# Optimization experiments

Measured on AMD Instinct MI355X. Metric: run time of the kernel, lower is better.

The kernel has to match this reference:

```python
import jax, jax.numpy as jnp
import numpy as np

B, C, Cs, CI, H, W = 4, 256, 256, 128, 64, 64

def setup_inputs() -> dict:
    key = jax.random.key(0)
    ks = jax.random.split(key, 9)
    sq = 1.0 / np.sqrt(C)
    ss = 1.0 / np.sqrt(Cs)
    return {
        "x_main": jax.random.normal(ks[0], (B, C, H, W), jnp.float32),
        "z_p": jax.random.normal(ks[1], (B, Cs, H, W), jnp.float32),
        "Wq": jax.random.normal(ks[2], (CI, C), jnp.float32) * sq,
        "bq": jax.random.normal(ks[3], (CI,), jnp.float32) * 0.01,
        "Wk": jax.random.normal(ks[4], (CI, Cs), jnp.float32) * ss,
        "bk": jax.random.normal(ks[5], (CI,), jnp.float32) * 0.01,
        "Wv": jax.random.normal(ks[6], (C, Cs), jnp.float32) * ss,
        "bv": jax.random.normal(ks[7], (C,), jnp.float32) * 0.01,
        "gamma": jax.random.normal(ks[8], (1,), jnp.float32) * 0.1,
    }

def reference(x_main, z_p, Wq, bq, Wk, bk, Wv, bv, gamma):
    b, c, h, w = x_main.shape
    n = h * w
    xm = x_main.reshape(b, c, n)          # [B, C, N]
    zf = z_p.reshape(b, z_p.shape[1], n)  # [B, Cs, M] (M == N here)
    # 1x1 convs == per-pixel channel projections
    q = jnp.einsum('oc,bcn->bon', Wq, xm) + bq[None, :, None]  # [B, CI, N]
    k = jnp.einsum('oc,bcm->bom', Wk, zf) + bk[None, :, None]  # [B, CI, M]
    v = jnp.einsum('oc,bcm->bom', Wv, zf) + bv[None, :, None]  # [B, C, M]
    # energy[b, n, m] = q_n . k_m  (no scaling, as in the original)
    energy = jnp.einsum('bcn,bcm->bnm', q, k)
    attention = jax.nn.softmax(energy, axis=-1)
    out = jnp.einsum('bom,bnm->bon', v, attention)  # [B, C, N]
    out = out.reshape(b, c, h, w)
    return gamma * out + x_main
```

## Files before the change

### kernel.cpp

```cpp
#include <hip/hip_runtime.h>
#include <hip/hip_bf16.h>


typedef __bf16  bf16x8  __attribute__((ext_vector_type(8)));
typedef float   f32x16  __attribute__((ext_vector_type(16)));

#define LOG2E 1.4426950408889634f

union BF8 { __hip_bfloat162 h[4]; bf16x8 v; };
union U4  { unsigned u[4]; bf16x8 v; };

__device__ inline bf16x8 pack8(const float f[8]) {
  BF8 u;
#pragma unroll
  for (int i = 0; i < 4; i++)
    u.h[i] = __float22bfloat162_rn(float2{f[2 * i], f[2 * i + 1]});
  return u.v;
}

__device__ inline void dma16(const void* g, void* l) {
  __builtin_amdgcn_global_load_lds(
      (const __attribute__((address_space(1))) unsigned int*)g,
      (__attribute__((address_space(3))) unsigned int*)l, 16, 0, 0);
}

__global__ __launch_bounds__(256) void prep_kernel(
    const float* __restrict__ x, const float* __restrict__ z,
    const float* __restrict__ Wq, const float* __restrict__ Wk,
    const float* __restrict__ Wv,
    __hip_bfloat16* __restrict__ xf, __hip_bfloat16* __restrict__ zf,
    __hip_bfloat16* __restrict__ wfr)
{
  __shared__ float lds[256 * 65];
  const int bi = blockIdx.x;
  const int tid = threadIdx.x;
  if (bi < 512) {
    const int sel = bi >> 8;
    const int b   = (bi >> 6) & 3;
    const int pc  = bi & 63;
    const float* in = sel ? z : x;
    __hip_bfloat16* outp = sel ? zf : xf;
    const size_t ib = (size_t)b * 256 * 4096 + pc * 64;
#pragma unroll 4
    for (int r = 0; r < 64; r++) {
      int ch = r * 4 + (tid >> 6);
      lds[ch * 65 + (tid & 63)] = in[ib + (size_t)ch * 4096 + (tid & 63)];
    }
    __syncthreads();
    const size_t ob = ((size_t)(b * 128 + pc * 2)) * 8192;
#pragma unroll
    for (int i = 0; i < 8; i++) {
      int c = i * 256 + tid;
      int grp = c >> 10, cs = (c >> 6) & 15, rem = c & 63;
      int hf = rem >> 5, l32 = rem & 31;
      float f[8];
      int chb = cs * 16 + hf * 8;
#pragma unroll
      for (int j = 0; j < 8; j++)
        f[j] = lds[(chb + j) * 65 + grp * 32 + l32];
      *(bf16x8*)(outp + ob + grp * 8192 + cs * 512 + hf * 256 + l32 * 8) =
          pack8(f);
    }
  } else {
    const int base = (bi - 512) * 4096;
#pragma unroll
    for (int i = 0; i < 16; i++) {
      int c = base + i * 256 + tid;
      const float* Ws; __hip_bfloat16* dst; int rc;
      if (c < 4096)      { Ws = Wq; dst = wfr;          rc = c; }
      else if (c < 8192) { Ws = Wk; dst = wfr + 32768;  rc = c - 4096; }
      else               { Ws = Wv; dst = wfr + 65536;  rc = c - 8192; }
      int ot = rc >> 10, cs = (rc >> 6) & 15, rem = rc & 63;
      int hf = rem >> 5, l32 = rem & 31;
      const float* src = Ws + (ot * 32 + l32) * 256 + cs * 16 + hf * 8;
      float f[8];
#pragma unroll
      for (int j = 0; j < 8; j++) f[j] = src[j];
      *(bf16x8*)(dst + ot * 8192 + cs * 512 + hf * 256 + l32 * 8) = pack8(f);
    }
  }
}

__global__ __launch_bounds__(256, 2) void proj_mfma(
    const __hip_bfloat16* __restrict__ xf, const __hip_bfloat16* __restrict__ zf,
    const __hip_bfloat16* __restrict__ wfr,
    const float* __restrict__ bq, const float* __restrict__ bk,
    const float* __restrict__ bv,
    __hip_bfloat16* __restrict__ qp, __hip_bfloat16* __restrict__ kp,
    __hip_bfloat16* __restrict__ vp)
{
  const int bi = blockIdx.x;
  int mode, b, pc, h = 0;
  if (bi < 256) { mode = bi >> 7; b = (bi >> 5) & 3; pc = bi & 31; }
  else { int j = bi - 256; mode = 2; b = j >> 6; pc = (j >> 1) & 31; h = j & 1; }
  const int tid = threadIdx.x, w = tid >> 6, lane = tid & 63,
            l32 = lane & 31, half = lane >> 5;

  const __hip_bfloat16* X = (mode == 0) ? xf : zf;
  const int wtile = (mode == 2 ? h * 4 : 0) + w;
  const int wbase = (mode == 0) ? 0 : (mode == 1) ? 32768 : 65536;
  const __hip_bfloat16* wp = wfr + wbase + wtile * 8192 + lane * 8;
  bf16x8 wfg[16];
#pragma unroll
  for (int cs = 0; cs < 16; cs++) wfg[cs] = *(const bf16x8*)(wp + cs * 512);

  const float* bias = (mode == 0) ? bq : (mode == 1) ? bk : bv;
  const int ochb = (mode == 2 ? h * 128 : 0) + w * 32;
  float bb[16];
#pragma unroll
  for (int r = 0; r < 16; r++)
    bb[r] = bias[ochb + (r & 3) + 8 * (r >> 2) + 4 * half];

  const int t4 = (l32 >> 2) & 3;
  const int kperm = (t4 == 1 || t4 == 2) ? (l32 ^ 12) : l32;

#pragma unroll 1
  for (int it = 0; it < 4; it++) {
    const int pg = pc * 4 + it;
    const __hip_bfloat16* xb = X + ((size_t)(b * 128 + pg)) * 8192 + lane * 8;
    f32x16 O = {};
#pragma unroll
    for (int cs = 0; cs < 16; cs++) {
      bf16x8 xr = *(const bf16x8*)(xb + cs * 512);
      O = __builtin_amdgcn_mfma_f32_32x32x16_bf16(wfg[cs], xr, O, 0, 0, 0);
    }
    if (mode == 0) {
      __hip_bfloat16* qb = qp + ((size_t)(b * 128 + pg)) * 4096;
#pragma unroll
      for (int r = 0; r < 16; r++) {
        int oc = ochb + (r & 3) + 8 * (r >> 2) + 4 * half;
        qb[(oc >> 4) * 512 + ((oc >> 3) & 1) * 256 + l32 * 8 + (oc & 7)] =
            __float2bfloat16((O[r] + bb[r]) * LOG2E);
      }
    } else if (mode == 1) {
      __hip_bfloat16* kb = kp + ((size_t)(b * 128 + pg)) * 4096;
#pragma unroll
      for (int r = 0; r < 16; r++) {
        int oc = ochb + (r & 3) + 8 * (r >> 2) + 4 * half;
        kb[(oc >> 4) * 512 + ((oc >> 3) & 1) * 256 + kperm * 8 + (oc & 7)] =
            __float2bfloat16(O[r] + bb[r]);
      }
    } else {
      __hip_bfloat16* vb = vp + ((size_t)(b * 128 + pg)) * 8192
          + (h * 4 + w) * 1024 + (l32 >> 4) * 512 + ((l32 >> 3) & 1) * 256
          + (l32 & 7);
#pragma unroll
      for (int r = 0; r < 16; r++) {
        int rr = (r & 3) + 8 * (r >> 2) + 4 * half;
        vb[rr * 8] = __float2bfloat16(O[r] + bb[r]);
      }
    }
  }
}

struct AttnSmem {
  union {
    __hip_bfloat16 kbuf[2][8192];
    float ostage[256][33];
  } u;
  float redu[4][32];
  float rinv[32];
};

__global__ __launch_bounds__(256, 3) void attn_kernel(
    const __hip_bfloat16* __restrict__ qv, const __hip_bfloat16* __restrict__ kv,
    const __hip_bfloat16* __restrict__ vv,
    const float* __restrict__ x_main, const float* __restrict__ gammap,
    float* __restrict__ out)
{
  __shared__ AttnSmem sm;
  const int i  = blockIdx.x;
  const int b  = (i & 7) >> 1;
  const int qt = ((i >> 3) << 1) | (i & 1);
  const int n0 = qt * 32;
  const int tid  = threadIdx.x;
  const int w    = tid >> 6, lane = tid & 63, l32 = lane & 31;
  const int kh   = w >> 1, chh = w & 1;

  bf16x8 qf[8];
  {
    const __hip_bfloat16* qb = qv + ((size_t)(b * 128 + qt)) * 4096 + lane * 8;
#pragma unroll
    for (int cs = 0; cs < 8; cs++) qf[cs] = *(const bf16x8*)(qb + cs * 512);
  }

  const __hip_bfloat16* kg = kv + (size_t)(b * 128) * 4096;
  const __hip_bfloat16* vg = vv + (size_t)(b * 128) * 8192;

  auto stage = [&](int t) {
    __hip_bfloat16* kd = sm.u.kbuf[t & 1];
    const __hip_bfloat16* ksrc = kg + (size_t)t * 8192 + lane * 8;
#pragma unroll
    for (int c = 0; c < 4; c++) {
      int ck = w * 4 + c;
      dma16(ksrc + ck * 512, kd + ck * 512 + lane * 8);
    }
  };

  f32x16 Oacc[4];
#pragma unroll
  for (int c = 0; c < 4; c++)
#pragma unroll
    for (int r = 0; r < 16; r++) Oacc[c][r] = 0.f;

  float l_lane = 0.f;

  auto qk_tile = [&](int t) -> f32x16 {
    const __hip_bfloat16* kbase = sm.u.kbuf[t & 1] + kh * 4096 + lane * 8;
    f32x16 S = {};
#pragma unroll
    for (int cs = 0; cs < 8; cs++) {
      bf16x8 kf = *(const bf16x8*)(kbase + cs * 512);
      S = __builtin_amdgcn_mfma_f32_32x32x16_bf16(kf, qf[cs], S, 0, 0, 0);
    }
    return S;
  };

  auto pv_tile = [&](int t, const f32x16& S) {
    unsigned p2[8];
    float s0 = 0.f, s1 = 0.f;
#pragma unroll
    for (int i2 = 0; i2 < 8; i2++) {
      float a = exp2f(S[2 * i2]     - 64.0f);
      float c = exp2f(S[2 * i2 + 1] - 64.0f);
      if (i2 & 1) s1 += a + c; else s0 += a + c;
      union { __hip_bfloat162 h; unsigned u; } cv;
      cv.h = __float22bfloat162_rn(float2{a, c});
      p2[i2] = cv.u;
    }
    l_lane += s0 + s1;
    U4 f0, f1;
    f0.u[0] = p2[0]; f0.u[1] = p2[1]; f0.u[2] = p2[2]; f0.u[3] = p2[3];
    f1.u[0] = p2[4]; f1.u[1] = p2[5]; f1.u[2] = p2[6]; f1.u[3] = p2[7];
    const bf16x8 pf0 = f0.v, pf1 = f1.v;
    const __hip_bfloat16* vb = vg + (size_t)(t * 2 + kh) * 8192
                             + chh * 4096 + lane * 8;
#pragma unroll
    for (int c = 0; c < 4; c++) {
      bf16x8 v0 = *(const bf16x8*)(vb + c * 1024);
      Oacc[c] = __builtin_amdgcn_mfma_f32_32x32x16_bf16(v0, pf0, Oacc[c], 0, 0, 0);
      bf16x8 v1 = *(const bf16x8*)(vb + c * 1024 + 512);
      Oacc[c] = __builtin_amdgcn_mfma_f32_32x32x16_bf16(v1, pf1, Oacc[c], 0, 0, 0);
    }
  };

  stage(0);
  __syncthreads();
  stage(1);
  {
    f32x16 S = qk_tile(0);
    pv_tile(0, S);
  }
#pragma unroll 1
  for (int t = 1; t < 64; ++t) {
    __syncthreads();
    if (t < 63) stage(t + 1);
    f32x16 S = qk_tile(t);
    pv_tile(t, S);
  }

  float lfull = l_lane + __shfl_xor(l_lane, 32);
  if (lane < 32) sm.redu[w][l32] = lfull;
  __syncthreads();
  const int hb = lane >> 5;
  if (kh == 0) {
#pragma unroll
    for (int c = 0; c < 4; c++) {
#pragma unroll
      for (int r = 0; r < 16; r++) {
        int ch = (chh * 4 + c) * 32 + (r & 3) + 8 * (r >> 2) + 4 * hb;
        sm.u.ostage[ch][l32] = Oacc[c][r];
      }
    }
  }
  if (tid < 32) sm.rinv[tid] = 1.0f / (sm.redu[0][tid] + sm.redu[2][tid]);
  __syncthreads();
  if (kh == 1) {
#pragma unroll
    for (int c = 0; c < 4; c++) {
#pragma unroll
      for (int r = 0; r < 16; r++) {
        int ch = (chh * 4 + c) * 32 + (r & 3) + 8 * (r >> 2) + 4 * hb;
        sm.u.ostage[ch][l32] += Oacc[c][r];
      }
    }
  }
  __syncthreads();

  const float gmm = gammap[0];
  const int pix = tid & 31;
  const float ri = sm.rinv[pix];
#pragma unroll
  for (int j = 0; j < 32; ++j) {
    int ch = (tid >> 5) * 32 + j;
    size_t g = ((size_t)(b * 256 + ch)) * 4096 + n0 + pix;
    out[g] = gmm * sm.u.ostage[ch][pix] * ri + x_main[g];
  }
}

extern "C" void kernel_launch(void* const* d_in, const int* in_sizes, int n_in,
                              void* d_out, int out_size, void* d_ws, size_t ws_size,
                              hipStream_t stream) {
  (void)in_sizes; (void)n_in; (void)out_size; (void)ws_size;
  const float* x  = (const float*)d_in[0];
  const float* z  = (const float*)d_in[1];
  const float* Wq = (const float*)d_in[2];
  const float* bq = (const float*)d_in[3];
  const float* Wk = (const float*)d_in[4];
  const float* bk = (const float*)d_in[5];
  const float* Wv = (const float*)d_in[6];
  const float* bv = (const float*)d_in[7];
  const float* gm = (const float*)d_in[8];
  float* out = (float*)d_out;

  char* ws = (char*)d_ws;
  const size_t MB = 1024 * 1024;
  __hip_bfloat16* qp  = (__hip_bfloat16*)(ws);
  __hip_bfloat16* kp  = (__hip_bfloat16*)(ws + 4 * MB);
  __hip_bfloat16* vp  = (__hip_bfloat16*)(ws + 8 * MB);
  __hip_bfloat16* xfp = (__hip_bfloat16*)(ws + 16 * MB);
  __hip_bfloat16* zfp = (__hip_bfloat16*)(ws + 24 * MB);
  __hip_bfloat16* wfp = (__hip_bfloat16*)(ws + 32 * MB);

  prep_kernel<<<516, 256, 0, stream>>>(x, z, Wq, Wk, Wv, xfp, zfp, wfp);
  proj_mfma  <<<512, 256, 0, stream>>>(xfp, zfp, wfp, bq, bk, bv, qp, kp, vp);
  attn_kernel<<<512, 256, 0, stream>>>(qp, kp, vp, x, gm, out);
}
```

Before: 215.4 us.

## Stage projection outputs in LDS for coalesced stores; register-prefetch K in attention

The projection kernel now writes its Q/K/V tiles into shared memory and then copies them out as contiguous 16-byte vector stores, replacing scattered 2-byte global stores. The attention kernel drops the LDS double-buffered K staging and its per-iteration barriers. Each wave instead loads its own K tile directly into registers, ping-ponging two register sets to prefetch the next tile, and loads V early in each iteration. This removes barrier and LDS traffic but raises register pressure, so launch bounds drop from 3 to 2 blocks per SM, which risks lower occupancy.

```diff
diff --git a/kernel.cpp b/kernel.cpp
--- a/kernel.cpp
+++ b/kernel.cpp
@@ -16,12 +16,6 @@
   for (int i = 0; i < 4; i++)
     u.h[i] = __float22bfloat162_rn(float2{f[2 * i], f[2 * i + 1]});
   return u.v;
-}
-
-__device__ inline void dma16(const void* g, void* l) {
-  __builtin_amdgcn_global_load_lds(
-      (const __attribute__((address_space(1))) unsigned int*)g,
-      (__attribute__((address_space(3))) unsigned int*)l, 16, 0, 0);
 }
 
 __global__ __launch_bounds__(256) void prep_kernel(
@@ -89,6 +83,7 @@
     __hip_bfloat16* __restrict__ qp, __hip_bfloat16* __restrict__ kp,
     __hip_bfloat16* __restrict__ vp)
 {
+  __shared__ __hip_bfloat16 st[4][4096];
   const int bi = blockIdx.x;
   int mode, b, pc, h = 0;
   if (bi < 256) { mode = bi >> 7; b = (bi >> 5) & 3; pc = bi & 31; }
@@ -124,45 +119,55 @@
       bf16x8 xr = *(const bf16x8*)(xb + cs * 512);
       O = __builtin_amdgcn_mfma_f32_32x32x16_bf16(wfg[cs], xr, O, 0, 0, 0);
     }
-    if (mode == 0) {
-      __hip_bfloat16* qb = qp + ((size_t)(b * 128 + pg)) * 4096;
+    if (mode != 2) {
 #pragma unroll
       for (int r = 0; r < 16; r++) {
-        int oc = ochb + (r & 3) + 8 * (r >> 2) + 4 * half;
-        qb[(oc >> 4) * 512 + ((oc >> 3) & 1) * 256 + l32 * 8 + (oc & 7)] =
-            __float2bfloat16((O[r] + bb[r]) * LOG2E);
+        int oc = w * 32 + (r & 3) + 8 * (r >> 2) + 4 * half;
+        float val = O[r] + bb[r];
+        if (mode == 0) val *= LOG2E;
+        int row = (mode == 1) ? kperm : l32;
+        st[it][(oc >> 4) * 512 + ((oc >> 3) & 1) * 256 + row * 8 + (oc & 7)] =
+            __float2bfloat16(val);
       }
-    } else if (mode == 1) {
-      __hip_bfloat16* kb = kp + ((size_t)(b * 128 + pg)) * 4096;
+    } else {
 #pragma unroll
       for (int r = 0; r < 16; r++) {
-        int oc = ochb + (r & 3) + 8 * (r >> 2) + 4 * half;
-        kb[(oc >> 4) * 512 + ((oc >> 3) & 1) * 256 + kperm * 8 + (oc & 7)] =
+        int ocr = w * 32 + (r & 3) + 8 * (r >> 2) + 4 * half;
+        st[it][(ocr >> 5) * 1024 + ((l32 >> 4) & 1) * 512 +
+               ((l32 >> 3) & 1) * 256 + (ocr & 31) * 8 + (l32 & 7)] =
             __float2bfloat16(O[r] + bb[r]);
       }
-    } else {
-      __hip_bfloat16* vb = vp + ((size_t)(b * 128 + pg)) * 8192
-          + (h * 4 + w) * 1024 + (l32 >> 4) * 512 + ((l32 >> 3) & 1) * 256
-          + (l32 & 7);
-#pragma unroll
-      for (int r = 0; r < 16; r++) {
-        int rr = (r & 3) + 8 * (r >> 2) + 4 * half;
-        vb[rr * 8] = __float2bfloat16(O[r] + bb[r]);
-      }
+    }
+  }
+  __syncthreads();
+
+  if (mode != 2) {
+    __hip_bfloat16* dst = (mode == 0 ? qp : kp)
+                        + ((size_t)(b * 128 + pc * 4)) * 4096;
+#pragma unroll
+    for (int i = 0; i < 8; i++) {
+      int c = i * 256 + tid;
+      *(bf16x8*)(dst + (size_t)c * 8) = *(const bf16x8*)&st[c >> 9][(c & 511) * 8];
+    }
+  } else {
+#pragma unroll
+    for (int i = 0; i < 8; i++) {
+      int c = i * 256 + tid;
+      int grp = c >> 9, rem = c & 511;
+      __hip_bfloat16* dst = vp + ((size_t)(b * 128 + pc * 4 + grp)) * 8192
+                          + h * 4096 + (size_t)rem * 8;
+      *(bf16x8*)dst = *(const bf16x8*)&st[grp][rem * 8];
     }
   }
 }
 
 struct AttnSmem {
-  union {
-    __hip_bfloat16 kbuf[2][8192];
-    float ostage[256][33];
-  } u;
+  float ostage[256][33];
   float redu[4][32];
   float rinv[32];
 };
 
-__global__ __launch_bounds__(256, 3) void attn_kernel(
+__global__ __launch_bounds__(256, 2) void attn_kernel(
     const __hip_bfloat16* __restrict__ qv, const __hip_bfloat16* __restrict__ kv,
     const __hip_bfloat16* __restrict__ vv,
     const float* __restrict__ x_main, const float* __restrict__ gammap,
@@ -184,79 +189,67 @@
     for (int cs = 0; cs < 8; cs++) qf[cs] = *(const bf16x8*)(qb + cs * 512);
   }
 
-  const __hip_bfloat16* kg = kv + (size_t)(b * 128) * 4096;
-  const __hip_bfloat16* vg = vv + (size_t)(b * 128) * 8192;
-
-  auto stage = [&](int t) {
-    __hip_bfloat16* kd = sm.u.kbuf[t & 1];
-    const __hip_bfloat16* ksrc = kg + (size_t)t * 8192 + lane * 8;
+  const __hip_bfloat16* kgh = kv + (size_t)(b * 128 + kh) * 4096 + lane * 8;
+  const __hip_bfloat16* vgh = vv + (size_t)(b * 128 + kh) * 8192
+                            + chh * 4096 + lane * 8;
+
+  f32x16 Oacc[4];
+#pragma unroll
+  for (int c = 0; c < 4; c++)
+#pragma unroll
+    for (int r = 0; r < 16; r++) Oacc[c][r] = 0.f;
+
+  float l_lane = 0.f;
+
+  bf16x8 KA[8], KB[8];
+#pragma unroll
+  for (int cs = 0; cs < 8; cs++) KA[cs] = *(const bf16x8*)(kgh + cs * 512);
+
+  auto body = [&](int t, bf16x8* Kc, bf16x8* Kn) {
+    const __hip_bfloat16* vb = vgh + (size_t)t * 16384;
+    bf16x8 Vc[8];
 #pragma unroll
     for (int c = 0; c < 4; c++) {
-      int ck = w * 4 + c;
-      dma16(ksrc + ck * 512, kd + ck * 512 + lane * 8);
-    }
-  };
-
-  f32x16 Oacc[4];
-#pragma unroll
-  for (int c = 0; c < 4; c++)
-#pragma unroll
-    for (int r = 0; r < 16; r++) Oacc[c][r] = 0.f;
-
-  float l_lane = 0.f;
-
-  auto qk_tile = [&](int t) -> f32x16 {
-    const __hip_bfloat16* kbase = sm.u.kbuf[t & 1] + kh * 4096 + lane * 8;
+      Vc[2 * c]     = *(const bf16x8*)(vb + c * 1024);
+      Vc[2 * c + 1] = *(const bf16x8*)(vb + c * 1024 + 512);
+    }
+    {
+      int tn = (t < 63) ? (t + 1) : 63;
+      const __hip_bfloat16* kb = kgh + (size_t)tn * 8192;
+#pragma unroll
+      for (int cs = 0; cs < 8; cs++) Kn[cs] = *(const bf16x8*)(kb + cs * 512);
+    }
     f32x16 S = {};
 #pragma unroll
-    for (int cs = 0; cs < 8; cs++) {
-      bf16x8 kf = *(const bf16x8*)(kbase + cs * 512);
-      S = __builtin_amdgcn_mfma_f32_32x32x16_bf16(kf, qf[cs], S, 0, 0, 0);
-    }
-    return S;
-  };
-
-  auto pv_tile = [&](int t, const f32x16& S) {
+    for (int cs = 0; cs < 8; cs++)
+      S = __builtin_amdgcn_mfma_f32_32x32x16_bf16(Kc[cs], qf[cs], S, 0, 0, 0);
     unsigned p2[8];
-    float s0 = 0.f, s1 = 0.f;
+    float lsub = 0.f;
 #pragma unroll
     for (int i2 = 0; i2 < 8; i2++) {
       float a = exp2f(S[2 * i2]     - 64.0f);
       float c = exp2f(S[2 * i2 + 1] - 64.0f);
-      if (i2 & 1) s1 += a + c; else s0 += a + c;
+      lsub += a + c;
       union { __hip_bfloat162 h; unsigned u; } cv;
       cv.h = __float22bfloat162_rn(float2{a, c});
       p2[i2] = cv.u;
     }
-    l_lane += s0 + s1;
+    l_lane += lsub;
     U4 f0, f1;
     f0.u[0] = p2[0]; f0.u[1] = p2[1]; f0.u[2] = p2[2]; f0.u[3] = p2[3];
     f1.u[0] = p2[4]; f1.u[1] = p2[5]; f1.u[2] = p2[6]; f1.u[3] = p2[7];
     const bf16x8 pf0 = f0.v, pf1 = f1.v;
-    const __hip_bfloat16* vb = vg + (size_t)(t * 2 + kh) * 8192
-                             + chh * 4096 + lane * 8;
 #pragma unroll
     for (int c = 0; c < 4; c++) {
-      bf16x8 v0 = *(const bf16x8*)(vb + c * 1024);
-      Oacc[c] = __builtin_amdgcn_mfma_f32_32x32x16_bf16(v0, pf0, Oacc[c], 0, 0, 0);
-      bf16x8 v1 = *(const bf16x8*)(vb + c * 1024 + 512);
-      Oacc[c] = __builtin_amdgcn_mfma_f32_32x32x16_bf16(v1, pf1, Oacc[c], 0, 0, 0);
+      Oacc[c] = __builtin_amdgcn_mfma_f32_32x32x16_bf16(Vc[2 * c],     pf0, Oacc[c], 0, 0, 0);
+      Oacc[c] = __builtin_amdgcn_mfma_f32_32x32x16_bf16(Vc[2 * c + 1], pf1, Oacc[c], 0, 0, 0);
     }
   };
 
-  stage(0);
-  __syncthreads();
-  stage(1);
-  {
-    f32x16 S = qk_tile(0);
-    pv_tile(0, S);
-  }
 #pragma unroll 1
-  for (int t = 1; t < 64; ++t) {
-    __syncthreads();
-    if (t < 63) stage(t + 1);
-    f32x16 S = qk_tile(t);
-    pv_tile(t, S);
+  for (int t = 0; t < 64; t += 2) {
+    body(t,     KA, KB);
+    body(t + 1, KB, KA);
   }
 
   float lfull = l_lane + __shfl_xor(l_lane, 32);
@@ -269,7 +262,7 @@
 #pragma unroll
       for (int r = 0; r < 16; r++) {
         int ch = (chh * 4 + c) * 32 + (r & 3) + 8 * (r >> 2) + 4 * hb;
-        sm.u.ostage[ch][l32] = Oacc[c][r];
+        sm.ostage[ch][l32] = Oacc[c][r];
       }
     }
   }
@@ -281,7 +274,7 @@
 #pragma unroll
       for (int r = 0; r < 16; r++) {
         int ch = (chh * 4 + c) * 32 + (r & 3) + 8 * (r >> 2) + 4 * hb;
-        sm.u.ostage[ch][l32] += Oacc[c][r];
+        sm.ostage[ch][l32] += Oacc[c][r];
       }
     }
   }
@@ -294,7 +287,7 @@
   for (int j = 0; j < 32; ++j) {
     int ch = (tid >> 5) * 32 + j;
     size_t g = ((size_t)(b * 256 + ch)) * 4096 + n0 + pix;
-    out[g] = gmm * sm.u.ostage[ch][pix] * ri + x_main[g];
+    out[g] = gmm * sm.ostage[ch][pix] * ri + x_main[g];
   }
 }
 
```

New measurement: 280.5 us. +30.2%, slower.

## Vectorize prep loads, pair projection tiles, stagger attention KV start, prefetch V

Applied to the files above, without the earlier changes.

The prep transpose now reads float4 per thread with a 68-float padded LDS row, in place of scalar loads with 65 padding. The projection kernel computes two pixel groups per iteration so each weight fragment feeds two MFMAs. The attention kernel rotates its starting key tile by query tile index, so concurrent blocks read different K/V tiles and spread L2/HBM traffic. It also issues all V global loads before the QK MFMAs to hide their latency. The costs are more live registers and a possible LDS bank-pattern change from the new padding.

```diff
diff --git a/kernel.cpp b/kernel.cpp
--- a/kernel.cpp
+++ b/kernel.cpp
@@ -31,7 +31,7 @@
     __hip_bfloat16* __restrict__ xf, __hip_bfloat16* __restrict__ zf,
     __hip_bfloat16* __restrict__ wfr)
 {
-  __shared__ float lds[256 * 65];
+  __shared__ float lds[256 * 68];
   const int bi = blockIdx.x;
   const int tid = threadIdx.x;
   if (bi < 512) {
@@ -41,10 +41,12 @@
     const float* in = sel ? z : x;
     __hip_bfloat16* outp = sel ? zf : xf;
     const size_t ib = (size_t)b * 256 * 4096 + pc * 64;
-#pragma unroll 4
-    for (int r = 0; r < 64; r++) {
-      int ch = r * 4 + (tid >> 6);
-      lds[ch * 65 + (tid & 63)] = in[ib + (size_t)ch * 4096 + (tid & 63)];
+    const int pix4 = (tid & 15) * 4;
+#pragma unroll
+    for (int it = 0; it < 16; it++) {
+      int ch = it * 16 + (tid >> 4);
+      float4 v4 = *(const float4*)&in[ib + (size_t)ch * 4096 + pix4];
+      *(float4*)&lds[ch * 68 + pix4] = v4;
     }
     __syncthreads();
     const size_t ob = ((size_t)(b * 128 + pc * 2)) * 8192;
@@ -57,7 +59,7 @@
       int chb = cs * 16 + hf * 8;
 #pragma unroll
       for (int j = 0; j < 8; j++)
-        f[j] = lds[(chb + j) * 65 + grp * 32 + l32];
+        f[j] = lds[(chb + j) * 68 + grp * 32 + l32];
       *(bf16x8*)(outp + ob + grp * 8192 + cs * 512 + hf * 256 + l32 * 8) =
           pack8(f);
     }
@@ -115,39 +117,47 @@
   const int kperm = (t4 == 1 || t4 == 2) ? (l32 ^ 12) : l32;
 
 #pragma unroll 1
-  for (int it = 0; it < 4; it++) {
-    const int pg = pc * 4 + it;
-    const __hip_bfloat16* xb = X + ((size_t)(b * 128 + pg)) * 8192 + lane * 8;
-    f32x16 O = {};
+  for (int itp = 0; itp < 2; itp++) {
+    const int pg0 = pc * 4 + itp * 2;
+    const __hip_bfloat16* xb0 = X + ((size_t)(b * 128 + pg0)) * 8192 + lane * 8;
+    const __hip_bfloat16* xb1 = xb0 + 8192;
+    f32x16 O0 = {}, O1 = {};
 #pragma unroll
     for (int cs = 0; cs < 16; cs++) {
-      bf16x8 xr = *(const bf16x8*)(xb + cs * 512);
-      O = __builtin_amdgcn_mfma_f32_32x32x16_bf16(wfg[cs], xr, O, 0, 0, 0);
-    }
-    if (mode == 0) {
-      __hip_bfloat16* qb = qp + ((size_t)(b * 128 + pg)) * 4096;
-#pragma unroll
-      for (int r = 0; r < 16; r++) {
-        int oc = ochb + (r & 3) + 8 * (r >> 2) + 4 * half;
-        qb[(oc >> 4) * 512 + ((oc >> 3) & 1) * 256 + l32 * 8 + (oc & 7)] =
-            __float2bfloat16((O[r] + bb[r]) * LOG2E);
-      }
-    } else if (mode == 1) {
-      __hip_bfloat16* kb = kp + ((size_t)(b * 128 + pg)) * 4096;
-#pragma unroll
-      for (int r = 0; r < 16; r++) {
-        int oc = ochb + (r & 3) + 8 * (r >> 2) + 4 * half;
-        kb[(oc >> 4) * 512 + ((oc >> 3) & 1) * 256 + kperm * 8 + (oc & 7)] =
-            __float2bfloat16(O[r] + bb[r]);
-      }
-    } else {
-      __hip_bfloat16* vb = vp + ((size_t)(b * 128 + pg)) * 8192
-          + (h * 4 + w) * 1024 + (l32 >> 4) * 512 + ((l32 >> 3) & 1) * 256
-          + (l32 & 7);
-#pragma unroll
-      for (int r = 0; r < 16; r++) {
-        int rr = (r & 3) + 8 * (r >> 2) + 4 * half;
-        vb[rr * 8] = __float2bfloat16(O[r] + bb[r]);
+      bf16x8 xr0 = *(const bf16x8*)(xb0 + cs * 512);
+      bf16x8 xr1 = *(const bf16x8*)(xb1 + cs * 512);
+      O0 = __builtin_amdgcn_mfma_f32_32x32x16_bf16(wfg[cs], xr0, O0, 0, 0, 0);
+      O1 = __builtin_amdgcn_mfma_f32_32x32x16_bf16(wfg[cs], xr1, O1, 0, 0, 0);
+    }
+#pragma unroll
+    for (int p = 0; p < 2; p++) {
+      const f32x16& O = p ? O1 : O0;
+      const int pg = pg0 + p;
+      if (mode == 0) {
+        __hip_bfloat16* qb = qp + ((size_t)(b * 128 + pg)) * 4096;
+#pragma unroll
+        for (int r = 0; r < 16; r++) {
+          int oc = ochb + (r & 3) + 8 * (r >> 2) + 4 * half;
+          qb[(oc >> 4) * 512 + ((oc >> 3) & 1) * 256 + l32 * 8 + (oc & 7)] =
+              __float2bfloat16((O[r] + bb[r]) * LOG2E);
+        }
+      } else if (mode == 1) {
+        __hip_bfloat16* kb = kp + ((size_t)(b * 128 + pg)) * 4096;
+#pragma unroll
+        for (int r = 0; r < 16; r++) {
+          int oc = ochb + (r & 3) + 8 * (r >> 2) + 4 * half;
+          kb[(oc >> 4) * 512 + ((oc >> 3) & 1) * 256 + kperm * 8 + (oc & 7)] =
+              __float2bfloat16(O[r] + bb[r]);
+        }
+      } else {
+        __hip_bfloat16* vb = vp + ((size_t)(b * 128 + pg)) * 8192
+            + (h * 4 + w) * 1024 + (l32 >> 4) * 512 + ((l32 >> 3) & 1) * 256
+            + (l32 & 7);
+#pragma unroll
+        for (int r = 0; r < 16; r++) {
+          int rr = (r & 3) + 8 * (r >> 2) + 4 * half;
+          vb[rr * 8] = __float2bfloat16(O[r] + bb[r]);
+        }
       }
     }
   }
@@ -176,6 +186,7 @@
   const int tid  = threadIdx.x;
   const int w    = tid >> 6, lane = tid & 63, l32 = lane & 31;
   const int kh   = w >> 1, chh = w & 1;
+  const int t0   = qt & 63;
 
   bf16x8 qf[8];
   {
@@ -187,9 +198,9 @@
   const __hip_bfloat16* kg = kv + (size_t)(b * 128) * 4096;
   const __hip_bfloat16* vg = vv + (size_t)(b * 128) * 8192;
 
-  auto stage = [&](int t) {
-    __hip_bfloat16* kd = sm.u.kbuf[t & 1];
-    const __hip_bfloat16* ksrc = kg + (size_t)t * 8192 + lane * 8;
+  auto stage = [&](int ta, int par) {
+    __hip_bfloat16* kd = sm.u.kbuf[par];
+    const __hip_bfloat16* ksrc = kg + (size_t)ta * 8192 + lane * 8;
 #pragma unroll
     for (int c = 0; c < 4; c++) {
       int ck = w * 4 + c;
@@ -205,58 +216,54 @@
 
   float l_lane = 0.f;
 
-  auto qk_tile = [&](int t) -> f32x16 {
-    const __hip_bfloat16* kbase = sm.u.kbuf[t & 1] + kh * 4096 + lane * 8;
+  auto body = [&](int par, int ta) {
+    const __hip_bfloat16* vb = vg + (size_t)(ta * 2 + kh) * 8192
+                             + chh * 4096 + lane * 8;
+    bf16x8 Vc[8];
+#pragma unroll
+    for (int c = 0; c < 4; c++) {
+      Vc[2 * c]     = *(const bf16x8*)(vb + c * 1024);
+      Vc[2 * c + 1] = *(const bf16x8*)(vb + c * 1024 + 512);
+    }
+    const __hip_bfloat16* kbase = sm.u.kbuf[par] + kh * 4096 + lane * 8;
     f32x16 S = {};
 #pragma unroll
     for (int cs = 0; cs < 8; cs++) {
       bf16x8 kf = *(const bf16x8*)(kbase + cs * 512);
       S = __builtin_amdgcn_mfma_f32_32x32x16_bf16(kf, qf[cs], S, 0, 0, 0);
     }
-    return S;
-  };
-
-  auto pv_tile = [&](int t, const f32x16& S) {
     unsigned p2[8];
-    float s0 = 0.f, s1 = 0.f;
+    float lsub = 0.f;
 #pragma unroll
     for (int i2 = 0; i2 < 8; i2++) {
       float a = exp2f(S[2 * i2]     - 64.0f);
       float c = exp2f(S[2 * i2 + 1] - 64.0f);
-      if (i2 & 1) s1 += a + c; else s0 += a + c;
+      lsub += a + c;
       union { __hip_bfloat162 h; unsigned u; } cv;
       cv.h = __float22bfloat162_rn(float2{a, c});
       p2[i2] = cv.u;
     }
-    l_lane += s0 + s1;
+    l_lane += lsub;
     U4 f0, f1;
     f0.u[0] = p2[0]; f0.u[1] = p2[1]; f0.u[2] = p2[2]; f0.u[3] = p2[3];
     f1.u[0] = p2[4]; f1.u[1] = p2[5]; f1.u[2] = p2[6]; f1.u[3] = p2[7];
     const bf16x8 pf0 = f0.v, pf1 = f1.v;
-    const __hip_bfloat16* vb = vg + (size_t)(t * 2 + kh) * 8192
-                             + chh * 4096 + lane * 8;
-#pragma unroll
-    for (int c = 0; c < 4; c++) {
-      bf16x8 v0 = *(const bf16x8*)(vb + c * 1024);
-      Oacc[c] = __builtin_amdgcn_mfma_f32_32x32x16_bf16(v0, pf0, Oacc[c], 0, 0, 0);
-      bf16x8 v1 = *(const bf16x8*)(vb + c * 1024 + 512);
-      Oacc[c] = __builtin_amdgcn_mfma_f32_32x32x16_bf16(v1, pf1, Oacc[c], 0, 0, 0);
+#pragma unroll
+    for (int c = 0; c < 4; c++) {
+      Oacc[c] = __builtin_amdgcn_mfma_f32_32x32x16_bf16(Vc[2 * c],     pf0, Oacc[c], 0, 0, 0);
+      Oacc[c] = __builtin_amdgcn_mfma_f32_32x32x16_bf16(Vc[2 * c + 1], pf1, Oacc[c], 0, 0, 0);
     }
   };
 
-  stage(0);
+  stage(t0, 0);
   __syncthreads();
-  stage(1);
-  {
-    f32x16 S = qk_tile(0);
-    pv_tile(0, S);
-  }
+  stage((t0 + 1) & 63, 1);
+  body(0, t0);
 #pragma unroll 1
-  for (int t = 1; t < 64; ++t) {
+  for (int lt = 1; lt < 64; ++lt) {
     __syncthreads();
-    if (t < 63) stage(t + 1);
-    f32x16 S = qk_tile(t);
-    pv_tile(t, S);
+    if (lt < 63) stage((lt + 1 + t0) & 63, (lt + 1) & 1);
+    body(lt & 1, (lt + t0) & 63);
   }
 
   float lfull = l_lane + __shfl_xor(l_lane, 32);
```

Measured after the change: 209.8 us. 1.03x faster.
